# Optimization experiments

Measured on AMD Instinct MI355X. Metric: run time of the kernel, lower is better.

Reference implementation:

```python
import jax, jax.numpy as jnp
import numpy as np

N, E, F, H, C = 50000, 800000, 128, 64, 40
EPS = 1e-12


def _l2norm(x):
    n = jnp.sqrt(jnp.sum(x * x, axis=-1, keepdims=True))
    return x / jnp.maximum(n, EPS)


def _sage_conv(x, edge_index, Wl, bl, Wr, num_nodes):
    # PyG SAGEConv, aggr='mean', normalize=True:
    #   out = lin_l(mean_{j in N(i)} x_j) + lin_r(x_i); out = l2_normalize(out)
    src, dst = edge_index[0], edge_index[1]
    msg = x[src]  # [E, F] gathered neighbor features
    agg = jax.ops.segment_sum(msg, dst, num_segments=num_nodes)
    cnt = jax.ops.segment_sum(jnp.ones((edge_index.shape[1],), x.dtype), dst,
                              num_segments=num_nodes)
    mean = agg / jnp.maximum(cnt, 1.0)[:, None]  # zero-in-degree nodes -> 0
    out = mean @ Wl + bl + x @ Wr
    return _l2norm(out)


def setup_inputs() -> dict:
    key = jax.random.key(0)
    ks = jax.random.split(key, 10)
    s = lambda fan_in: 1.0 / np.sqrt(fan_in)
    x = jax.random.normal(ks[0], (N, F), dtype=jnp.float32)
    edge_index = jax.random.randint(ks[1], (2, E), 0, N, dtype=jnp.int64)
    # conv1: SAGEConv(F -> H); lin_l has bias, lin_r has no bias
    Wl1 = jax.random.uniform(ks[2], (F, H), jnp.float32, -s(F), s(F))
    bl1 = jnp.zeros((H,), jnp.float32)
    Wr1 = jax.random.uniform(ks[3], (F, H), jnp.float32, -s(F), s(F))
    # lin1: Linear(F + H -> H)
    Wlin = jax.random.uniform(ks[4], (F + H, H), jnp.float32, -s(F + H), s(F + H))
    blin = jax.random.uniform(ks[5], (H,), jnp.float32, -s(F + H), s(F + H))
    # conv2: SAGEConv(H -> C)
    Wl2 = jax.random.uniform(ks[6], (H, C), jnp.float32, -s(H), s(H))
    bl2 = jnp.zeros((C,), jnp.float32)
    Wr2 = jax.random.uniform(ks[7], (H, C), jnp.float32, -s(H), s(H))
    return {"x": x, "edge_index": edge_index,
            "Wl1": Wl1, "bl1": bl1, "Wr1": Wr1,
            "Wlin": Wlin, "blin": blin,
            "Wl2": Wl2, "bl2": bl2, "Wr2": Wr2}


def reference(x, edge_index, Wl1, bl1, Wr1, Wlin, blin, Wl2, bl2, Wr2):
    hidden = jax.nn.relu(_sage_conv(x, edge_index, Wl1, bl1, Wr1, N))
    h = jax.nn.relu(jnp.concatenate([x, hidden], axis=1) @ Wlin + blin)
    # dropout is identity in eval mode
    out = _sage_conv(h, edge_index, Wl2, bl2, Wr2, N)
    return out
```

## Files before the change

### kernel.cpp

```cpp
#include <hip/hip_runtime.h>

static constexpr int NN = 50000;
static constexpr int NE = 800000;
static constexpr int F  = 128;
static constexpr int H  = 64;
static constexpr int C  = 40;

static constexpr int NB_BK = 8;
static constexpr int NCH   = 32;
static constexpr int ECH   = NE / NCH;
static constexpr int NBK   = NN / NB_BK;

typedef __attribute__((ext_vector_type(8))) short bf16x8;
typedef __attribute__((ext_vector_type(4))) float f32x4;

__device__ inline unsigned short f2bf(float f) {
  unsigned int u = __builtin_bit_cast(unsigned int, f);
  u = (u + 0x7fff + ((u >> 16) & 1)) >> 16;
  return (unsigned short)u;
}


__global__ __launch_bounds__(256) void k_hist(const int* __restrict__ ei,
                                              int* __restrict__ hist) {
  __shared__ int cnt[NBK];
  int i = blockIdx.x & 7;
  int j = blockIdx.x >> 3;
  for (int t = threadIdx.x; t < NBK; t += 256) cnt[t] = 0;
  __syncthreads();
  int lo = i * NBK;
  const int* dst = ei + NE + j * ECH;
  for (int base = threadIdx.x * 4; base < ECH; base += 256 * 4) {
    int4 d4 = *reinterpret_cast<const int4*>(dst + base);
    if ((unsigned)(d4.x - lo) < (unsigned)NBK) atomicAdd(&cnt[d4.x - lo], 1);
    if ((unsigned)(d4.y - lo) < (unsigned)NBK) atomicAdd(&cnt[d4.y - lo], 1);
    if ((unsigned)(d4.z - lo) < (unsigned)NBK) atomicAdd(&cnt[d4.z - lo], 1);
    if ((unsigned)(d4.w - lo) < (unsigned)NBK) atomicAdd(&cnt[d4.w - lo], 1);
  }
  __syncthreads();
  int* hrow = hist + (size_t)j * NN + lo;
  for (int t = threadIdx.x; t < NBK; t += 256) hrow[t] = cnt[t];
}

__global__ __launch_bounds__(256) void k_scan(int* __restrict__ hist,
                                              int* __restrict__ deg,
                                              int* __restrict__ start,
                                              int* __restrict__ counter) {
  int lane = threadIdx.x & 63;
  int wid  = (blockIdx.x * blockDim.x + threadIdx.x) >> 6;
  int nw   = (gridDim.x * blockDim.x) >> 6;
  int nchunks = (NN + 63) >> 6;
  for (int c = wid; c < nchunks; c += nw) {
    int n = (c << 6) + lane;
    int d = 0;
    if (n < NN) {
      int run = 0;
#pragma unroll
      for (int j = 0; j < NCH; ++j) {
        int v = hist[(size_t)j * NN + n];
        hist[(size_t)j * NN + n] = run;
        run += v;
      }
      d = run;
    }
    int inc = d;
#pragma unroll
    for (int off = 1; off < 64; off <<= 1) {
      int t = __shfl_up(inc, off, 64);
      if (lane >= off) inc += t;
    }
    int total = __shfl(inc, 63, 64);
    int base = 0;
    if (lane == 63) base = atomicAdd(counter, total);
    base = __shfl(base, 63, 64);
    if (n < NN) {
      deg[n]   = d;
      start[n] = base + inc - d;
    }
  }
}

__global__ __launch_bounds__(256) void k_fill2(const int* __restrict__ ei,
                                               const int* __restrict__ hist,
                                               const int* __restrict__ start,
                                               int* __restrict__ csr_src) {
  __shared__ int fill[NBK];
  int i = blockIdx.x & 7;
  int j = blockIdx.x >> 3;
  int lo = i * NBK;
  const int* hrow = hist + (size_t)j * NN + lo;
  for (int t = threadIdx.x; t < NBK; t += 256) fill[t] = start[lo + t] + hrow[t];
  __syncthreads();
  const int* srcp = ei + j * ECH;
  const int* dstp = ei + NE + j * ECH;
  for (int base = threadIdx.x * 4; base < ECH; base += 256 * 4) {
    int4 s4 = *reinterpret_cast<const int4*>(srcp + base);
    int4 d4 = *reinterpret_cast<const int4*>(dstp + base);
    if ((unsigned)(d4.x - lo) < (unsigned)NBK) { int p = atomicAdd(&fill[d4.x - lo], 1); csr_src[p] = s4.x; }
    if ((unsigned)(d4.y - lo) < (unsigned)NBK) { int p = atomicAdd(&fill[d4.y - lo], 1); csr_src[p] = s4.y; }
    if ((unsigned)(d4.z - lo) < (unsigned)NBK) { int p = atomicAdd(&fill[d4.z - lo], 1); csr_src[p] = s4.z; }
    if ((unsigned)(d4.w - lo) < (unsigned)NBK) { int p = atomicAdd(&fill[d4.w - lo], 1); csr_src[p] = s4.w; }
  }
}


__global__ __launch_bounds__(256) void k_cvt(const float* __restrict__ x,
                                             unsigned short* __restrict__ xb) {
  int stride = gridDim.x * blockDim.x;
  for (int i = blockIdx.x * blockDim.x + threadIdx.x; i < NN * F / 4; i += stride) {
    float4 v = reinterpret_cast<const float4*>(x)[i];
    ushort4 o = {f2bf(v.x), f2bf(v.y), f2bf(v.z), f2bf(v.w)};
    reinterpret_cast<ushort4*>(xb)[i] = o;
  }
}


__device__ inline void packW(const float* __restrict__ W, int J, int NT,
                             unsigned short* __restrict__ Wf, int idx) {
  int j  = idx & 7;
  int l  = (idx >> 3) & 63;
  int nt = (idx >> 9) % NT;
  int s  = idx / (512 * NT);
  int k  = s * 32 + (l >> 4) * 8 + j;
  int n  = nt * 16 + (l & 15);
  float v = (n < J) ? W[k * J + n] : 0.f;
  Wf[idx] = f2bf(v);
}

__global__ __launch_bounds__(256) void k_prep(const float* __restrict__ Wl1,
                                              const float* __restrict__ Wr1,
                                              const float* __restrict__ Wlin,
                                              const float* __restrict__ Wl2,
                                              const float* __restrict__ Wr2,
                                              unsigned short* __restrict__ Wf1l,
                                              unsigned short* __restrict__ Wf1r,
                                              unsigned short* __restrict__ Wflin,
                                              unsigned short* __restrict__ Wf2l,
                                              unsigned short* __restrict__ Wf2r) {
  int id0 = blockIdx.x * blockDim.x + threadIdx.x;
  int ns  = gridDim.x * blockDim.x;
  for (int i = id0; i < 4 * 4 * 512; i += ns) packW(Wl1, 64, 4, Wf1l, i);
  for (int i = id0; i < 4 * 4 * 512; i += ns) packW(Wr1, 64, 4, Wf1r, i);
  for (int i = id0; i < 6 * 4 * 512; i += ns) packW(Wlin, 64, 4, Wflin, i);
  for (int i = id0; i < 2 * 3 * 512; i += ns) packW(Wl2, 40, 3, Wf2l, i);
  for (int i = id0; i < 2 * 3 * 512; i += ns) packW(Wr2, 40, 3, Wf2r, i);
}


template <int K1, int K2, int JOUT, int NT, int NMAT, bool BIAS, bool RELU, bool OUTBF>
__global__ __launch_bounds__(256) void k_mf(const unsigned short* __restrict__ A1,
                                            const unsigned short* __restrict__ A2,
                                            const unsigned short* __restrict__ Wf0,
                                            const unsigned short* __restrict__ Wf1,
                                            const float* __restrict__ bias,
                                            void* __restrict__ Y0v,
                                            void* __restrict__ Y1v) {
  constexpr int K   = K1 + K2;
  constexpr int NKS = K / 32;
  int lane = threadIdx.x & 63;
  int w    = __builtin_amdgcn_readfirstlane(threadIdx.x >> 6);
  int m    = lane & 15;
  int kg   = lane >> 4;
  int n0   = blockIdx.x * 64;
  int row  = n0 + w * 16 + m;
  int rowc = row < NN ? row : NN - 1;

  f32x4 acc[NMAT][NT];
#pragma unroll
  for (int mt = 0; mt < NMAT; ++mt)
#pragma unroll
    for (int nt = 0; nt < NT; ++nt) acc[mt][nt] = {0.f, 0.f, 0.f, 0.f};

#pragma unroll
  for (int s = 0; s < NKS; ++s) {
    const unsigned short* Ab; int rs, koff;
    if (s * 32 < K1) { Ab = A1; rs = K1; koff = s * 32; }
    else             { Ab = A2; rs = K2; koff = s * 32 - K1; }
    bf16x8 a = *reinterpret_cast<const bf16x8*>(Ab + (size_t)rowc * rs + koff + kg * 8);
#pragma unroll
    for (int mt = 0; mt < NMAT; ++mt) {
      const unsigned short* Wf = (NMAT == 2 && mt) ? Wf1 : Wf0;
#pragma unroll
      for (int nt = 0; nt < NT; ++nt) {
        bf16x8 b = *reinterpret_cast<const bf16x8*>(Wf + (size_t)((s * NT + nt) * 64 + lane) * 8);
        acc[mt][nt] = __builtin_amdgcn_mfma_f32_16x16x32_bf16(a, b, acc[mt][nt], 0, 0, 0);
      }
    }
  }

#pragma unroll
  for (int mt = 0; mt < NMAT; ++mt) {
    void* Yv = (NMAT == 2 && mt) ? Y1v : Y0v;
#pragma unroll
    for (int nt = 0; nt < NT; ++nt) {
      int gc = nt * 16 + m;
      bool cv = gc < JOUT;
      float bb = (BIAS && cv) ? bias[gc] : 0.f;
#pragma unroll
      for (int r = 0; r < 4; ++r) {
        int grow = n0 + w * 16 + kg * 4 + r;
        if (grow < NN && cv) {
          float v = acc[mt][nt][r] + bb;
          if (RELU) v = fmaxf(v, 0.f);
          if (OUTBF) ((unsigned short*)Yv)[(size_t)grow * JOUT + gc] = f2bf(v);
          else       ((float*)Yv)[(size_t)grow * JOUT + gc] = v;
        }
      }
    }
  }
}


template <int JC, bool RELU, bool OUTBF>
__global__ __launch_bounds__(256) void k_agg(const float* __restrict__ p,
                                             const float* __restrict__ q,
                                             const float* __restrict__ bl,
                                             const int* __restrict__ deg,
                                             const int* __restrict__ start,
                                             const int* __restrict__ csr_src,
                                             void* __restrict__ outp) {
  int lane = threadIdx.x & 63;
  int wid  = (blockIdx.x * blockDim.x + threadIdx.x) >> 6;
  int nw   = (gridDim.x * blockDim.x) >> 6;
  bool jl = lane < JC;
  int lidx = jl ? lane : 0;
  for (int node = wid; node < NN; node += nw) {
    int d  = __builtin_amdgcn_readfirstlane(deg[node]);
    int st = __builtin_amdgcn_readfirstlane(start[node]);
    float a0 = 0.f, a1 = 0.f, a2 = 0.f, a3 = 0.f;
    float a4 = 0.f, a5 = 0.f, a6 = 0.f, a7 = 0.f;
    int t = 0;
    for (; t + 8 <= d; t += 8) {
      int s0 = __builtin_amdgcn_readfirstlane(csr_src[st + t + 0]);
      int s1 = __builtin_amdgcn_readfirstlane(csr_src[st + t + 1]);
      int s2 = __builtin_amdgcn_readfirstlane(csr_src[st + t + 2]);
      int s3 = __builtin_amdgcn_readfirstlane(csr_src[st + t + 3]);
      int s4 = __builtin_amdgcn_readfirstlane(csr_src[st + t + 4]);
      int s5 = __builtin_amdgcn_readfirstlane(csr_src[st + t + 5]);
      int s6 = __builtin_amdgcn_readfirstlane(csr_src[st + t + 6]);
      int s7 = __builtin_amdgcn_readfirstlane(csr_src[st + t + 7]);
      a0 += p[(size_t)s0 * JC + lidx];
      a1 += p[(size_t)s1 * JC + lidx];
      a2 += p[(size_t)s2 * JC + lidx];
      a3 += p[(size_t)s3 * JC + lidx];
      a4 += p[(size_t)s4 * JC + lidx];
      a5 += p[(size_t)s5 * JC + lidx];
      a6 += p[(size_t)s6 * JC + lidx];
      a7 += p[(size_t)s7 * JC + lidx];
    }
    if (t + 4 <= d) {
      int s0 = __builtin_amdgcn_readfirstlane(csr_src[st + t + 0]);
      int s1 = __builtin_amdgcn_readfirstlane(csr_src[st + t + 1]);
      int s2 = __builtin_amdgcn_readfirstlane(csr_src[st + t + 2]);
      int s3 = __builtin_amdgcn_readfirstlane(csr_src[st + t + 3]);
      a0 += p[(size_t)s0 * JC + lidx];
      a1 += p[(size_t)s1 * JC + lidx];
      a2 += p[(size_t)s2 * JC + lidx];
      a3 += p[(size_t)s3 * JC + lidx];
      t += 4;
    }
    for (; t < d; ++t) {
      int s = __builtin_amdgcn_readfirstlane(csr_src[st + t]);
      a0 += p[(size_t)s * JC + lidx];
    }
    float acc = ((a0 + a1) + (a2 + a3)) + ((a4 + a5) + (a6 + a7));
    float mean = acc / fmaxf((float)d, 1.0f);
    float v = 0.f;
    if (jl) v = mean + bl[lidx] + q[(size_t)node * JC + lidx];
    float ss = v * v;
#pragma unroll
    for (int off = 32; off > 0; off >>= 1) ss += __shfl_xor(ss, off, 64);
    v = v / fmaxf(sqrtf(ss), 1e-12f);
    if (RELU) v = fmaxf(v, 0.f);
    if (jl) {
      if (OUTBF) ((unsigned short*)outp)[(size_t)node * JC + lidx] = f2bf(v);
      else       ((float*)outp)[(size_t)node * JC + lidx] = v;
    }
  }
}


static inline size_t align256(size_t x) { return (x + 255) & ~(size_t)255; }

extern "C" void kernel_launch(void* const* d_in, const int* in_sizes, int n_in,
                              void* d_out, int out_size, void* d_ws, size_t ws_size,
                              hipStream_t stream) {
  const float* x    = (const float*)d_in[0];
  const int*   ei   = (const int*)d_in[1];
  const float* Wl1  = (const float*)d_in[2];
  const float* bl1  = (const float*)d_in[3];
  const float* Wr1  = (const float*)d_in[4];
  const float* Wlin = (const float*)d_in[5];
  const float* blin = (const float*)d_in[6];
  const float* Wl2  = (const float*)d_in[7];
  const float* bl2  = (const float*)d_in[8];
  const float* Wr2  = (const float*)d_in[9];
  float* out = (float*)d_out;

  char* w = (char*)d_ws;
  size_t off = 0;
  int* deg     = (int*)(w + off); off += align256((size_t)NN * 4);
  int* start   = (int*)(w + off); off += align256((size_t)NN * 4);
  int* counter = (int*)(w + off); off += 256;
  int* csr_src = (int*)(w + off); off += align256((size_t)NE * 4);
  int* hist    = (int*)(w + off); off += align256((size_t)NCH * NN * 4);
  unsigned short* xb      = (unsigned short*)(w + off); off += align256((size_t)NN * F * 2);
  unsigned short* hiddenb = (unsigned short*)(w + off); off += align256((size_t)NN * H * 2);
  unsigned short* hb      = (unsigned short*)(w + off); off += align256((size_t)NN * H * 2);
  float* p1 = (float*)(w + off); off += align256((size_t)NN * H * 4);
  float* q1 = (float*)(w + off); off += align256((size_t)NN * H * 4);
  float* p2 = (float*)(w + off); off += align256((size_t)NN * C * 4);
  float* q2 = (float*)(w + off); off += align256((size_t)NN * C * 4);
  unsigned short* Wf1l  = (unsigned short*)(w + off); off += align256(4 * 4 * 512 * 2);
  unsigned short* Wf1r  = (unsigned short*)(w + off); off += align256(4 * 4 * 512 * 2);
  unsigned short* Wflin = (unsigned short*)(w + off); off += align256(6 * 4 * 512 * 2);
  unsigned short* Wf2l  = (unsigned short*)(w + off); off += align256(2 * 3 * 512 * 2);
  unsigned short* Wf2r  = (unsigned short*)(w + off); off += align256(2 * 3 * 512 * 2);

  hipMemsetAsync(counter, 0, 4, stream);

  const int T = 256;
  const int NT64 = (NN + 63) / 64;

  k_hist <<<NB_BK * NCH, T, 0, stream>>>(ei, hist);
  k_scan <<<196, T, 0, stream>>>(hist, deg, start, counter);
  k_fill2<<<NB_BK * NCH, T, 0, stream>>>(ei, hist, start, csr_src);

  k_cvt <<<782, T, 0, stream>>>(x, xb);
  k_prep<<<48, T, 0, stream>>>(Wl1, Wr1, Wlin, Wl2, Wr2, Wf1l, Wf1r, Wflin, Wf2l, Wf2r);

  k_mf<F, 0, H, 4, 2, false, false, false><<<NT64, T, 0, stream>>>(
      xb, nullptr, Wf1l, Wf1r, nullptr, p1, q1);

  k_agg<H, true, true><<<2048, T, 0, stream>>>(p1, q1, bl1, deg, start, csr_src, hiddenb);

  k_mf<F, H, H, 4, 1, true, true, true><<<NT64, T, 0, stream>>>(
      xb, hiddenb, Wflin, nullptr, blin, hb, nullptr);

  k_mf<H, 0, C, 3, 2, false, false, false><<<NT64, T, 0, stream>>>(
      hb, nullptr, Wf2l, Wf2r, nullptr, p2, q2);

  k_agg<C, false, false><<<2048, T, 0, stream>>>(p2, q2, bl2, deg, start, csr_src, out);
}
```

Baseline: 232.3 us.

## Merge independent launches, store projections in bf16, widen gather unroll

Independent stages now share launches by dispatching on block index: histogram with the x conversion, scan with weight packing, and CSR fill with the first projection GEMM. This cuts the launch count and drops the memset, since block 0 now zeroes the counter. The p/q projection buffers change from fp32 to bf16, halving the bytes gathered in aggregation, and the gather loop is unrolled to 16 edges to keep more loads in flight. Storing in bf16 adds rounding error to the neighbour sums. The counter reset now relies on hist blocks running before k_p2 in stream order.

After: 209.3 us. 9.9% less time.

```diff
diff --git a/kernel.cpp b/kernel.cpp
--- a/kernel.cpp
+++ b/kernel.cpp
@@ -10,6 +10,8 @@
 static constexpr int NCH   = 32;
 static constexpr int ECH   = NE / NCH;
 static constexpr int NBK   = NN / NB_BK;
+static constexpr int NCSR  = NB_BK * NCH;
+static constexpr int NT64  = (NN + 63) / 64;
 
 typedef __attribute__((ext_vector_type(8))) short bf16x8;
 typedef __attribute__((ext_vector_type(4))) float f32x4;
@@ -19,15 +21,19 @@
   u = (u + 0x7fff + ((u >> 16) & 1)) >> 16;
   return (unsigned short)u;
 }
-
-
-__global__ __launch_bounds__(256) void k_hist(const int* __restrict__ ei,
-                                              int* __restrict__ hist) {
+__device__ inline float bf2f(unsigned short u) {
+  return __builtin_bit_cast(float, (unsigned int)u << 16);
+}
+
+
+__device__ void hist_body(int bid, const int* __restrict__ ei,
+                          int* __restrict__ hist, int* __restrict__ counter) {
   __shared__ int cnt[NBK];
-  int i = blockIdx.x & 7;
-  int j = blockIdx.x >> 3;
+  int i = bid & 7;
+  int j = bid >> 3;
   for (int t = threadIdx.x; t < NBK; t += 256) cnt[t] = 0;
   __syncthreads();
+  if (bid == 0 && threadIdx.x == 0) *counter = 0;
   int lo = i * NBK;
   const int* dst = ei + NE + j * ECH;
   for (int base = threadIdx.x * 4; base < ECH; base += 256 * 4) {
@@ -42,51 +48,87 @@
   for (int t = threadIdx.x; t < NBK; t += 256) hrow[t] = cnt[t];
 }
 
-__global__ __launch_bounds__(256) void k_scan(int* __restrict__ hist,
-                                              int* __restrict__ deg,
-                                              int* __restrict__ start,
-                                              int* __restrict__ counter) {
+__device__ void cvt_body(int bid, const float* __restrict__ x,
+                         unsigned short* __restrict__ xb) {
+  int id = bid * 256 + threadIdx.x;
+  int ns = NT64 * 256;
+  for (int i = id; i < NN * F / 4; i += ns) {
+    float4 v = reinterpret_cast<const float4*>(x)[i];
+    ushort4 o = {f2bf(v.x), f2bf(v.y), f2bf(v.z), f2bf(v.w)};
+    reinterpret_cast<ushort4*>(xb)[i] = o;
+  }
+}
+
+__device__ void scan_body(int bid, int* __restrict__ hist,
+                          int* __restrict__ deg, int* __restrict__ start,
+                          int* __restrict__ counter) {
   int lane = threadIdx.x & 63;
-  int wid  = (blockIdx.x * blockDim.x + threadIdx.x) >> 6;
-  int nw   = (gridDim.x * blockDim.x) >> 6;
+  int wid  = (bid * 256 + threadIdx.x) >> 6;
   int nchunks = (NN + 63) >> 6;
-  for (int c = wid; c < nchunks; c += nw) {
-    int n = (c << 6) + lane;
-    int d = 0;
-    if (n < NN) {
-      int run = 0;
-#pragma unroll
-      for (int j = 0; j < NCH; ++j) {
-        int v = hist[(size_t)j * NN + n];
-        hist[(size_t)j * NN + n] = run;
-        run += v;
-      }
-      d = run;
-    }
-    int inc = d;
-#pragma unroll
-    for (int off = 1; off < 64; off <<= 1) {
-      int t = __shfl_up(inc, off, 64);
-      if (lane >= off) inc += t;
-    }
-    int total = __shfl(inc, 63, 64);
-    int base = 0;
-    if (lane == 63) base = atomicAdd(counter, total);
-    base = __shfl(base, 63, 64);
-    if (n < NN) {
-      deg[n]   = d;
-      start[n] = base + inc - d;
-    }
-  }
-}
-
-__global__ __launch_bounds__(256) void k_fill2(const int* __restrict__ ei,
-                                               const int* __restrict__ hist,
-                                               const int* __restrict__ start,
-                                               int* __restrict__ csr_src) {
+  if (wid >= nchunks) return;
+  int n = (wid << 6) + lane;
+  int d = 0;
+  if (n < NN) {
+    int run = 0;
+#pragma unroll
+    for (int j = 0; j < NCH; ++j) {
+      int v = hist[(size_t)j * NN + n];
+      hist[(size_t)j * NN + n] = run;
+      run += v;
+    }
+    d = run;
+  }
+  int inc = d;
+#pragma unroll
+  for (int off = 1; off < 64; off <<= 1) {
+    int t = __shfl_up(inc, off, 64);
+    if (lane >= off) inc += t;
+  }
+  int total = __shfl(inc, 63, 64);
+  int base = 0;
+  if (lane == 63) base = atomicAdd(counter, total);
+  base = __shfl(base, 63, 64);
+  if (n < NN) {
+    deg[n]   = d;
+    start[n] = base + inc - d;
+  }
+}
+
+__device__ inline void packW(const float* __restrict__ W, int J, int NT,
+                             unsigned short* __restrict__ Wf, int idx) {
+  int j  = idx & 7;
+  int l  = (idx >> 3) & 63;
+  int nt = (idx >> 9) % NT;
+  int s  = idx / (512 * NT);
+  int k  = s * 32 + (l >> 4) * 8 + j;
+  int n  = nt * 16 + (l & 15);
+  float v = (n < J) ? W[k * J + n] : 0.f;
+  Wf[idx] = f2bf(v);
+}
+
+__device__ void prep_body(int bid,
+                          const float* __restrict__ Wl1, const float* __restrict__ Wr1,
+                          const float* __restrict__ Wlin,
+                          const float* __restrict__ Wl2, const float* __restrict__ Wr2,
+                          unsigned short* __restrict__ Wf1l, unsigned short* __restrict__ Wf1r,
+                          unsigned short* __restrict__ Wflin,
+                          unsigned short* __restrict__ Wf2l, unsigned short* __restrict__ Wf2r) {
+  int id0 = bid * 256 + threadIdx.x;
+  int ns  = 48 * 256;
+  for (int i = id0; i < 4 * 4 * 512; i += ns) packW(Wl1, 64, 4, Wf1l, i);
+  for (int i = id0; i < 4 * 4 * 512; i += ns) packW(Wr1, 64, 4, Wf1r, i);
+  for (int i = id0; i < 6 * 4 * 512; i += ns) packW(Wlin, 64, 4, Wflin, i);
+  for (int i = id0; i < 2 * 3 * 512; i += ns) packW(Wl2, 40, 3, Wf2l, i);
+  for (int i = id0; i < 2 * 3 * 512; i += ns) packW(Wr2, 40, 3, Wf2r, i);
+}
+
+__device__ void fill2_body(int bid, const int* __restrict__ ei,
+                           const int* __restrict__ hist,
+                           const int* __restrict__ start,
+                           int* __restrict__ csr_src) {
   __shared__ int fill[NBK];
-  int i = blockIdx.x & 7;
-  int j = blockIdx.x >> 3;
+  int i = bid & 7;
+  int j = bid >> 3;
   int lo = i * NBK;
   const int* hrow = hist + (size_t)j * NN + lo;
   for (int t = threadIdx.x; t < NBK; t += 256) fill[t] = start[lo + t] + hrow[t];
@@ -104,64 +146,21 @@
 }
 
 
-__global__ __launch_bounds__(256) void k_cvt(const float* __restrict__ x,
-                                             unsigned short* __restrict__ xb) {
-  int stride = gridDim.x * blockDim.x;
-  for (int i = blockIdx.x * blockDim.x + threadIdx.x; i < NN * F / 4; i += stride) {
-    float4 v = reinterpret_cast<const float4*>(x)[i];
-    ushort4 o = {f2bf(v.x), f2bf(v.y), f2bf(v.z), f2bf(v.w)};
-    reinterpret_cast<ushort4*>(xb)[i] = o;
-  }
-}
-
-
-__device__ inline void packW(const float* __restrict__ W, int J, int NT,
-                             unsigned short* __restrict__ Wf, int idx) {
-  int j  = idx & 7;
-  int l  = (idx >> 3) & 63;
-  int nt = (idx >> 9) % NT;
-  int s  = idx / (512 * NT);
-  int k  = s * 32 + (l >> 4) * 8 + j;
-  int n  = nt * 16 + (l & 15);
-  float v = (n < J) ? W[k * J + n] : 0.f;
-  Wf[idx] = f2bf(v);
-}
-
-__global__ __launch_bounds__(256) void k_prep(const float* __restrict__ Wl1,
-                                              const float* __restrict__ Wr1,
-                                              const float* __restrict__ Wlin,
-                                              const float* __restrict__ Wl2,
-                                              const float* __restrict__ Wr2,
-                                              unsigned short* __restrict__ Wf1l,
-                                              unsigned short* __restrict__ Wf1r,
-                                              unsigned short* __restrict__ Wflin,
-                                              unsigned short* __restrict__ Wf2l,
-                                              unsigned short* __restrict__ Wf2r) {
-  int id0 = blockIdx.x * blockDim.x + threadIdx.x;
-  int ns  = gridDim.x * blockDim.x;
-  for (int i = id0; i < 4 * 4 * 512; i += ns) packW(Wl1, 64, 4, Wf1l, i);
-  for (int i = id0; i < 4 * 4 * 512; i += ns) packW(Wr1, 64, 4, Wf1r, i);
-  for (int i = id0; i < 6 * 4 * 512; i += ns) packW(Wlin, 64, 4, Wflin, i);
-  for (int i = id0; i < 2 * 3 * 512; i += ns) packW(Wl2, 40, 3, Wf2l, i);
-  for (int i = id0; i < 2 * 3 * 512; i += ns) packW(Wr2, 40, 3, Wf2r, i);
-}
-
-
 template <int K1, int K2, int JOUT, int NT, int NMAT, bool BIAS, bool RELU, bool OUTBF>
-__global__ __launch_bounds__(256) void k_mf(const unsigned short* __restrict__ A1,
-                                            const unsigned short* __restrict__ A2,
-                                            const unsigned short* __restrict__ Wf0,
-                                            const unsigned short* __restrict__ Wf1,
-                                            const float* __restrict__ bias,
-                                            void* __restrict__ Y0v,
-                                            void* __restrict__ Y1v) {
+__device__ void mf_body(int bid,
+                        const unsigned short* __restrict__ A1,
+                        const unsigned short* __restrict__ A2,
+                        const unsigned short* __restrict__ Wf0,
+                        const unsigned short* __restrict__ Wf1,
+                        const float* __restrict__ bias,
+                        void* __restrict__ Y0v, void* __restrict__ Y1v) {
   constexpr int K   = K1 + K2;
   constexpr int NKS = K / 32;
   int lane = threadIdx.x & 63;
   int w    = __builtin_amdgcn_readfirstlane(threadIdx.x >> 6);
   int m    = lane & 15;
   int kg   = lane >> 4;
-  int n0   = blockIdx.x * 64;
+  int n0   = bid * 64;
   int row  = n0 + w * 16 + m;
   int rowc = row < NN ? row : NN - 1;
 
@@ -211,9 +210,60 @@
 }
 
 
+__global__ __launch_bounds__(256) void k_p1(const int* __restrict__ ei,
+                                            int* __restrict__ hist,
+                                            int* __restrict__ counter,
+                                            const float* __restrict__ x,
+                                            unsigned short* __restrict__ xb) {
+  if (blockIdx.x < NCSR) hist_body(blockIdx.x, ei, hist, counter);
+  else                   cvt_body(blockIdx.x - NCSR, x, xb);
+}
+
+__global__ __launch_bounds__(256) void k_p2(int* __restrict__ hist,
+                                            int* __restrict__ deg,
+                                            int* __restrict__ start,
+                                            int* __restrict__ counter,
+                                            const float* Wl1, const float* Wr1,
+                                            const float* Wlin,
+                                            const float* Wl2, const float* Wr2,
+                                            unsigned short* Wf1l, unsigned short* Wf1r,
+                                            unsigned short* Wflin,
+                                            unsigned short* Wf2l, unsigned short* Wf2r) {
+  if (blockIdx.x < 196) scan_body(blockIdx.x, hist, deg, start, counter);
+  else prep_body(blockIdx.x - 196, Wl1, Wr1, Wlin, Wl2, Wr2,
+                 Wf1l, Wf1r, Wflin, Wf2l, Wf2r);
+}
+
+__global__ __launch_bounds__(256) void k_p3(const int* __restrict__ ei,
+                                            const int* __restrict__ hist,
+                                            const int* __restrict__ start,
+                                            int* __restrict__ csr_src,
+                                            const unsigned short* __restrict__ xb,
+                                            const unsigned short* __restrict__ Wf1l,
+                                            const unsigned short* __restrict__ Wf1r,
+                                            unsigned short* __restrict__ p1b,
+                                            unsigned short* __restrict__ q1b) {
+  if (blockIdx.x < NCSR) fill2_body(blockIdx.x, ei, hist, start, csr_src);
+  else mf_body<F, 0, H, 4, 2, false, false, true>(blockIdx.x - NCSR, xb, nullptr,
+                                                  Wf1l, Wf1r, nullptr, p1b, q1b);
+}
+
+template <int K1, int K2, int JOUT, int NT, int NMAT, bool BIAS, bool RELU, bool OUTBF>
+__global__ __launch_bounds__(256) void k_mf(const unsigned short* __restrict__ A1,
+                                            const unsigned short* __restrict__ A2,
+                                            const unsigned short* __restrict__ Wf0,
+                                            const unsigned short* __restrict__ Wf1,
+                                            const float* __restrict__ bias,
+                                            void* __restrict__ Y0v,
+                                            void* __restrict__ Y1v) {
+  mf_body<K1, K2, JOUT, NT, NMAT, BIAS, RELU, OUTBF>(blockIdx.x, A1, A2, Wf0, Wf1,
+                                                     bias, Y0v, Y1v);
+}
+
+
 template <int JC, bool RELU, bool OUTBF>
-__global__ __launch_bounds__(256) void k_agg(const float* __restrict__ p,
-                                             const float* __restrict__ q,
+__global__ __launch_bounds__(256) void k_agg(const unsigned short* __restrict__ p,
+                                             const unsigned short* __restrict__ q,
                                              const float* __restrict__ bl,
                                              const int* __restrict__ deg,
                                              const int* __restrict__ start,
@@ -227,46 +277,42 @@
   for (int node = wid; node < NN; node += nw) {
     int d  = __builtin_amdgcn_readfirstlane(deg[node]);
     int st = __builtin_amdgcn_readfirstlane(start[node]);
-    float a0 = 0.f, a1 = 0.f, a2 = 0.f, a3 = 0.f;
-    float a4 = 0.f, a5 = 0.f, a6 = 0.f, a7 = 0.f;
+    float acc8[8];
+#pragma unroll
+    for (int i = 0; i < 8; ++i) acc8[i] = 0.f;
     int t = 0;
-    for (; t + 8 <= d; t += 8) {
+    for (; t + 16 <= d; t += 16) {
+      int s[16];
+#pragma unroll
+      for (int i = 0; i < 16; ++i)
+        s[i] = __builtin_amdgcn_readfirstlane(csr_src[st + t + i]);
+      unsigned short v[16];
+#pragma unroll
+      for (int i = 0; i < 16; ++i) v[i] = p[(size_t)s[i] * JC + lidx];
+#pragma unroll
+      for (int i = 0; i < 16; ++i) acc8[i & 7] += bf2f(v[i]);
+    }
+    for (; t + 4 <= d; t += 4) {
       int s0 = __builtin_amdgcn_readfirstlane(csr_src[st + t + 0]);
       int s1 = __builtin_amdgcn_readfirstlane(csr_src[st + t + 1]);
       int s2 = __builtin_amdgcn_readfirstlane(csr_src[st + t + 2]);
       int s3 = __builtin_amdgcn_readfirstlane(csr_src[st + t + 3]);
-      int s4 = __builtin_amdgcn_readfirstlane(csr_src[st + t + 4]);
-      int s5 = __builtin_amdgcn_readfirstlane(csr_src[st + t + 5]);
-      int s6 = __builtin_amdgcn_readfirstlane(csr_src[st + t + 6]);
-      int s7 = __builtin_amdgcn_readfirstlane(csr_src[st + t + 7]);
-      a0 += p[(size_t)s0 * JC + lidx];
-      a1 += p[(size_t)s1 * JC + lidx];
-      a2 += p[(size_t)s2 * JC + lidx];
-      a3 += p[(size_t)s3 * JC + lidx];
-      a4 += p[(size_t)s4 * JC + lidx];
-      a5 += p[(size_t)s5 * JC + lidx];
-      a6 += p[(size_t)s6 * JC + lidx];
-      a7 += p[(size_t)s7 * JC + lidx];
-    }
-    if (t + 4 <= d) {
-      int s0 = __builtin_amdgcn_readfirstlane(csr_src[st + t + 0]);
-      int s1 = __builtin_amdgcn_readfirstlane(csr_src[st + t + 1]);
-      int s2 = __builtin_amdgcn_readfirstlane(csr_src[st + t + 2]);
-      int s3 = __builtin_amdgcn_readfirstlane(csr_src[st + t + 3]);
-      a0 += p[(size_t)s0 * JC + lidx];
-      a1 += p[(size_t)s1 * JC + lidx];
-      a2 += p[(size_t)s2 * JC + lidx];
-      a3 += p[(size_t)s3 * JC + lidx];
-      t += 4;
+      unsigned short v0 = p[(size_t)s0 * JC + lidx];
+      unsigned short v1 = p[(size_t)s1 * JC + lidx];
+      unsigned short v2 = p[(size_t)s2 * JC + lidx];
+      unsigned short v3 = p[(size_t)s3 * JC + lidx];
+      acc8[0] += bf2f(v0); acc8[1] += bf2f(v1);
+      acc8[2] += bf2f(v2); acc8[3] += bf2f(v3);
     }
     for (; t < d; ++t) {
       int s = __builtin_amdgcn_readfirstlane(csr_src[st + t]);
-      a0 += p[(size_t)s * JC + lidx];
-    }
-    float acc = ((a0 + a1) + (a2 + a3)) + ((a4 + a5) + (a6 + a7));
+      acc8[0] += bf2f(p[(size_t)s * JC + lidx]);
+    }
+    float acc = ((acc8[0] + acc8[1]) + (acc8[2] + acc8[3])) +
+                ((acc8[4] + acc8[5]) + (acc8[6] + acc8[7]));
     float mean = acc / fmaxf((float)d, 1.0f);
     float v = 0.f;
-    if (jl) v = mean + bl[lidx] + q[(size_t)node * JC + lidx];
+    if (jl) v = mean + bl[lidx] + bf2f(q[(size_t)node * JC + lidx]);
     float ss = v * v;
 #pragma unroll
     for (int off = 32; off > 0; off >>= 1) ss += __shfl_xor(ss, off, 64);
@@ -307,38 +353,28 @@
   unsigned short* xb      = (unsigned short*)(w + off); off += align256((size_t)NN * F * 2);
   unsigned short* hiddenb = (unsigned short*)(w + off); off += align256((size_t)NN * H * 2);
   unsigned short* hb      = (unsigned short*)(w + off); off += align256((size_t)NN * H * 2);
-  float* p1 = (float*)(w + off); off += align256((size_t)NN * H * 4);
-  float* q1 = (float*)(w + off); off += align256((size_t)NN * H * 4);
-  float* p2 = (float*)(w + off); off += align256((size_t)NN * C * 4);
-  float* q2 = (float*)(w + off); off += align256((size_t)NN * C * 4);
+  unsigned short* p1b = (unsigned short*)(w + off); off += align256((size_t)NN * H * 2);
+  unsigned short* q1b = (unsigned short*)(w + off); off += align256((size_t)NN * H * 2);
+  unsigned short* p2b = (unsigned short*)(w + off); off += align256((size_t)NN * C * 2);
+  unsigned short* q2b = (unsigned short*)(w + off); off += align256((size_t)NN * C * 2);
   unsigned short* Wf1l  = (unsigned short*)(w + off); off += align256(4 * 4 * 512 * 2);
   unsigned short* Wf1r  = (unsigned short*)(w + off); off += align256(4 * 4 * 512 * 2);
   unsigned short* Wflin = (unsigned short*)(w + off); off += align256(6 * 4 * 512 * 2);
   unsigned short* Wf2l  = (unsigned short*)(w + off); off += align256(2 * 3 * 512 * 2);
   unsigned short* Wf2r  = (unsigned short*)(w + off); off += align256(2 * 3 * 512 * 2);
 
-  hipMemsetAsync(counter, 0, 4, stream);
-
   const int T = 256;
-  const int NT64 = (NN + 63) / 64;
-
-  k_hist <<<NB_BK * NCH, T, 0, stream>>>(ei, hist);
-  k_scan <<<196, T, 0, stream>>>(hist, deg, start, counter);
-  k_fill2<<<NB_BK * NCH, T, 0, stream>>>(ei, hist, start, csr_src);
-
-  k_cvt <<<782, T, 0, stream>>>(x, xb);
-  k_prep<<<48, T, 0, stream>>>(Wl1, Wr1, Wlin, Wl2, Wr2, Wf1l, Wf1r, Wflin, Wf2l, Wf2r);
-
-  k_mf<F, 0, H, 4, 2, false, false, false><<<NT64, T, 0, stream>>>(
-      xb, nullptr, Wf1l, Wf1r, nullptr, p1, q1);
-
-  k_agg<H, true, true><<<2048, T, 0, stream>>>(p1, q1, bl1, deg, start, csr_src, hiddenb);
-
+
+  k_p1<<<NCSR + NT64, T, 0, stream>>>(ei, hist, counter, x, xb);
+  k_p2<<<244, T, 0, stream>>>(hist, deg, start, counter,
+                              Wl1, Wr1, Wlin, Wl2, Wr2,
+                              Wf1l, Wf1r, Wflin, Wf2l, Wf2r);
+  k_p3<<<NCSR + NT64, T, 0, stream>>>(ei, hist, start, csr_src,
+                                      xb, Wf1l, Wf1r, p1b, q1b);
+  k_agg<H, true, true><<<2048, T, 0, stream>>>(p1b, q1b, bl1, deg, start, csr_src, hiddenb);
   k_mf<F, H, H, 4, 1, true, true, true><<<NT64, T, 0, stream>>>(
       xb, hiddenb, Wflin, nullptr, blin, hb, nullptr);
-
-  k_mf<H, 0, C, 3, 2, false, false, false><<<NT64, T, 0, stream>>>(
-      hb, nullptr, Wf2l, Wf2r, nullptr, p2, q2);
-
-  k_agg<C, false, false><<<2048, T, 0, stream>>>(p2, q2, bl2, deg, start, csr_src, out);
-}
+  k_mf<H, 0, C, 3, 2, false, false, true><<<NT64, T, 0, stream>>>(
+      hb, nullptr, Wf2l, Wf2r, nullptr, p2b, q2b);
+  k_agg<C, false, false><<<2048, T, 0, stream>>>(p2b, q2b, bl2, deg, start, csr_src, out);
+}
```
